# Optimization experiments

Hardware: AMD Instinct MI355X
Metric: run time of the kernel (lower is better)

The kernel has to match this reference:

```python
import jax, jax.numpy as jnp
import numpy as np

N = 40000          # spots (nodes)
G = 3000           # genes (input features)
C = 20             # num_classes
E = N * 16         # edges (avg degree 16)


def _uniform(key, shape, stdv):
    return jax.random.uniform(key, shape, jnp.float32, -stdv, stdv)


def _linear_params(key, n_in, n_out):
    # torch Linear default init: U(-1/sqrt(in), 1/sqrt(in)); stored as [in, out]
    k1, k2 = jax.random.split(key)
    s = 1.0 / np.sqrt(n_in)
    return _uniform(k1, (n_in, n_out), s), _uniform(k2, (n_out,), s)


def setup_inputs() -> dict:
    key = jax.random.key(0)
    ks = jax.random.split(key, 32)
    x = jax.random.normal(ks[0], (N, G), jnp.float32)
    adj_rows = jax.random.randint(ks[1], (E,), 0, N, jnp.int32)
    adj_cols = jax.random.randint(ks[2], (E,), 0, N, jnp.int32)
    adj_vals = jax.random.uniform(ks[3], (E,), jnp.float32)

    # GCN weights: GraphConvolution init U(-1/sqrt(out), 1/sqrt(out)), no bias
    def gcn_w(k, fi, fo):
        return _uniform(k, (fi, fo), 1.0 / np.sqrt(fo))

    inp = {
        "x": x, "adj_rows": adj_rows, "adj_cols": adj_cols, "adj_vals": adj_vals,
        "W1": gcn_w(ks[4], G, 512), "W2": gcn_w(ks[5], 512, 256),
        "W3": gcn_w(ks[6], 256, 128), "W4": gcn_w(ks[7], 128, 128),
        "W5": gcn_w(ks[8], 128, C),
    }
    # AE linear layers
    for name, (fi, fo), k in [
        ("enc1", (G, 512), ks[9]), ("enc2", (512, 256), ks[10]),
        ("enc3", (256, 128), ks[11]), ("zl", (128, 128), ks[12]),
        ("dec1", (128, 128), ks[13]), ("dec2", (128, 256), ks[14]),
        ("dec3", (256, 512), ks[15]), ("xbar", (512, G), ks[16]),
    ]:
        w, b = _linear_params(k, fi, fo)
        inp[name + "_w"], inp[name + "_b"] = w, b
    # Attention projection vectors (Linear(in_size, 1, bias=False))
    inp["a1"] = _uniform(ks[17], (512,), 1.0 / np.sqrt(512))
    inp["a2"] = _uniform(ks[18], (256,), 1.0 / np.sqrt(256))
    inp["a3"] = _uniform(ks[19], (128,), 1.0 / np.sqrt(128))
    inp["a4"] = _uniform(ks[20], (128,), 1.0 / np.sqrt(128))
    inp["scale"] = jax.random.normal(ks[21], (G,), jnp.float32)
    inp["additive"] = jax.random.normal(ks[22], (G,), jnp.float32)
    return inp


def _spmm(rows, cols, vals, dense, n):
    # out[r] = sum_e vals[e] * dense[cols[e]] for rows[e]==r  (sparse [n,n] @ dense)
    return jax.ops.segment_sum(vals[:, None] * dense[cols], rows, num_segments=n)


def _gcn(x, rows, cols, vals, W, n, active=True):
    out = _spmm(rows, cols, vals, x @ W, n)
    return jax.nn.relu(out) if active else out


def _attn(h, t, a):
    # stack two [N,D] branches, softmax over the branch axis, weighted sum
    z = jnp.stack([h, t], axis=1)           # [N,2,D]
    w = jnp.einsum('nbd,d->nb', z, a)        # [N,2]
    beta = jax.nn.softmax(w, axis=1)
    return jnp.einsum('nb,nbd->nd', beta, z)


def reference(x, adj_rows, adj_cols, adj_vals,
              W1, W2, W3, W4, W5,
              enc1_w, enc1_b, enc2_w, enc2_b, enc3_w, enc3_b, zl_w, zl_b,
              dec1_w, dec1_b, dec2_w, dec2_b, dec3_w, dec3_b, xbar_w, xbar_b,
              a1, a2, a3, a4, scale, additive):
    n = x.shape[0]
    # autoencoder
    t1 = jax.nn.relu(x @ enc1_w + enc1_b)
    t2 = jax.nn.relu(t1 @ enc2_w + enc2_b)
    t3 = jax.nn.relu(t2 @ enc3_w + enc3_b)
    z = t3 @ zl_w + zl_b
    d1 = jax.nn.relu(z @ dec1_w + dec1_b)
    d2 = jax.nn.relu(d1 @ dec2_w + dec2_b)
    d3 = jax.nn.relu(d2 @ dec3_w + dec3_b)
    x_bar = d3 @ xbar_w + xbar_b
    # GCN stack with attention-fused AE skip connections
    h = _gcn(x, adj_rows, adj_cols, adj_vals, W1, n)
    emb = _attn(h, t1, a1)
    h = _gcn(emb, adj_rows, adj_cols, adj_vals, W2, n)
    emb = _attn(h, t2, a2)
    h = _gcn(emb, adj_rows, adj_cols, adj_vals, W3, n)
    emb = _attn(h, t3, a3)
    h = _gcn(emb, adj_rows, adj_cols, adj_vals, W4, n)
    emb = _attn(h, z, a4)
    output = _gcn(emb, adj_rows, adj_cols, adj_vals, W5, n, active=False)
    return output, x_bar, jax.nn.sigmoid(scale), jnp.exp(additive)
```

## Files before the change

### kernel.cpp

```cpp
#include <hip/hip_runtime.h>
#include <cmath>

typedef unsigned short u16;
typedef unsigned int u32;
typedef __attribute__((ext_vector_type(8))) short short8;
typedef __attribute__((ext_vector_type(4))) short short4v;
typedef __attribute__((ext_vector_type(4))) float f32x4;

__device__ __forceinline__ float bf2f(u16 h) {
  union { u32 u; float f; } v; v.u = ((u32)h) << 16; return v.f;
}
__device__ __forceinline__ u16 f2bf(float f) {
  union { float f; u32 u; } v; v.f = f;
  u32 u = v.u;
  u32 r = (u + 0x7FFFu + ((u >> 16) & 1u)) >> 16;
  return (u16)r;
}

__global__ void convx_kernel(const float* __restrict__ x, u16* __restrict__ A0) {
  int idx = blockIdx.x * 256 + threadIdx.x;
  int r = blockIdx.y;
  if (idx >= 752) return;
  short4v o;
  if (r < 40000 && idx < 750) {
    float4 v = *(const float4*)(x + (size_t)r * 3000 + idx * 4);
    o[0] = (short)f2bf(v.x); o[1] = (short)f2bf(v.y);
    o[2] = (short)f2bf(v.z); o[3] = (short)f2bf(v.w);
  } else {
    o[0] = 0; o[1] = 0; o[2] = 0; o[3] = 0;
  }
  *(short4v*)(A0 + (size_t)r * 3008 + idx * 4) = o;
}

__global__ void convw_kernel(const float* __restrict__ W, u16* __restrict__ Wt,
                             int K, int N, int Kp) {
  int k = blockIdx.x * 256 + threadIdx.x;
  int n = blockIdx.y;
  if (k >= Kp) return;
  float v = (k < K && n < N) ? W[(size_t)k * N + n] : 0.f;
  Wt[(size_t)n * Kp + k] = f2bf(v);
}

__global__ void zero_kernel(int* p, int n) {
  int i = blockIdx.x * 256 + threadIdx.x;
  if (i < n) p[i] = 0;
}
__global__ void count_kernel(const int* __restrict__ rows, int* __restrict__ counts, int E) {
  int i = blockIdx.x * 256 + threadIdx.x;
  if (i < E) atomicAdd(&counts[rows[i]], 1);
}
__global__ __launch_bounds__(1024) void scan_kernel(const int* __restrict__ counts,
                                                    int* __restrict__ rowptr,
                                                    int* __restrict__ cursor, int n) {
  __shared__ int buf[1024];
  __shared__ int carry_s;
  int tid = threadIdx.x;
  if (tid == 0) carry_s = 0;
  __syncthreads();
  for (int base = 0; base < n; base += 1024) {
    int i = base + tid;
    int v = (i < n) ? counts[i] : 0;
    buf[tid] = v;
    __syncthreads();
    for (int off = 1; off < 1024; off <<= 1) {
      int tv = (tid >= off) ? buf[tid - off] : 0;
      __syncthreads();
      buf[tid] += tv;
      __syncthreads();
    }
    int incl = buf[tid];
    int carry = carry_s;
    if (i < n) { int ex = carry + incl - v; rowptr[i] = ex; cursor[i] = ex; }
    __syncthreads();
    if (tid == 1023) carry_s = carry + incl;
    __syncthreads();
  }
  if (tid == 0) rowptr[n] = carry_s;
}
__global__ void scatter_kernel(const int* __restrict__ rows, const int* __restrict__ cols,
                               const float* __restrict__ vals, int* __restrict__ cursor,
                               int* __restrict__ cols_s, float* __restrict__ vals_s, int E) {
  int i = blockIdx.x * 256 + threadIdx.x;
  if (i < E) {
    int r = rows[i];
    int p = atomicAdd(&cursor[r], 1);
    cols_s[p] = cols[i];
    vals_s[p] = vals[i];
  }
}

#define BM 128
#define BN 128
#define BK 32

template <bool BIAS, bool RELU, bool OUTBF16, int CH>
__global__ __launch_bounds__(256, 2) void gemm_bf16(
    const u16* __restrict__ A, int lda, const u16* __restrict__ Bt, int ldb,
    void* __restrict__ C1, int ldc,
    const float* __restrict__ bias, int M, int Nreal, int K, int MT, int NT) {
  __shared__ __align__(16) u16 As[2][BM * BK];
  __shared__ __align__(16) u16 Bs[2][BN * BK];
  const int lin = blockIdx.x;
  const int per = CH * NT;
  const int g = lin / per;
  const int r0 = lin - g * per;
  const int bx0 = g * CH;
  const int cw = min(CH, MT - bx0);
  const int bx = bx0 + r0 % cw;
  const int by = r0 / cw;

  const int tid = threadIdx.x;
  const int lane = tid & 63;
  const int wave = tid >> 6;
  const int mblk = bx * BM;
  const int nblk = by * BN;
  const int wm = (wave & 1) * 64;
  const int wn = (wave >> 1) * 64;
  const int ml = lane & 15;
  const int kg = lane >> 4;

  f32x4 acc[4][4];
#pragma unroll
  for (int i = 0; i < 4; ++i)
#pragma unroll
    for (int j = 0; j < 4; ++j) acc[i][j] = (f32x4)(0.f);

  const int nk = K / BK;
  const int sr = tid >> 2;
  const int sc = (tid & 3) * 8;
  const u16* gA0 = A + (size_t)(mblk + sr) * lda + sc;
  const u16* gA1 = A + (size_t)(mblk + sr + 64) * lda + sc;
  const u16* gB0 = Bt + (size_t)(nblk + sr) * ldb + sc;
  const u16* gB1 = Bt + (size_t)(nblk + sr + 64) * ldb + sc;

  auto stage = [&](int buf, int kt) {
    const int ko = kt * BK;
    u16* lA = &As[buf][0] + wave * 512;
    u16* lB = &Bs[buf][0] + wave * 512;
    __builtin_amdgcn_global_load_lds((const void*)(gA0 + ko), (void*)lA, 16, 0, 0);
    __builtin_amdgcn_global_load_lds((const void*)(gA1 + ko), (void*)(lA + 2048), 16, 0, 0);
    __builtin_amdgcn_global_load_lds((const void*)(gB0 + ko), (void*)lB, 16, 0, 0);
    __builtin_amdgcn_global_load_lds((const void*)(gB1 + ko), (void*)(lB + 2048), 16, 0, 0);
  };

  stage(0, 0);
  asm volatile("s_waitcnt vmcnt(0)" ::: "memory");
  __syncthreads();

  int cur = 0;
  for (int kt = 0; kt < nk; ++kt) {
    if (kt + 1 < nk) stage(cur ^ 1, kt + 1);
    short8 af[4], bfr[4];
#pragma unroll
    for (int i = 0; i < 4; ++i) {
      af[i] = *(const short8*)&As[cur][(wm + i * 16 + ml) * BK + kg * 8];
      bfr[i] = *(const short8*)&Bs[cur][(wn + i * 16 + ml) * BK + kg * 8];
    }
#pragma unroll
    for (int i = 0; i < 4; ++i)
#pragma unroll
      for (int j = 0; j < 4; ++j)
        acc[i][j] = __builtin_amdgcn_mfma_f32_16x16x32_bf16(af[i], bfr[j], acc[i][j], 0, 0, 0);
    asm volatile("s_waitcnt vmcnt(0)" ::: "memory");
    __syncthreads();
    cur ^= 1;
  }

#pragma unroll
  for (int i = 0; i < 4; ++i) {
    const int row0 = mblk + wm + i * 16 + kg * 4;
#pragma unroll
    for (int j = 0; j < 4; ++j) {
      const int col = nblk + wn + j * 16 + ml;
      if (col < Nreal) {
        float bv = BIAS ? bias[col] : 0.f;
#pragma unroll
        for (int r = 0; r < 4; ++r) {
          const int row = row0 + r;
          if (row < M) {
            float v = acc[i][j][r] + bv;
            if (RELU) v = fmaxf(v, 0.f);
            if (OUTBF16)
              ((u16*)C1)[(size_t)row * ldc + col] = f2bf(v);
            else
              ((float*)C1)[(size_t)row * ldc + col] = v;
          }
        }
      }
    }
  }
}

template <int MODE>
__global__ __launch_bounds__(512, 1) void gemm256p(
    const u16* __restrict__ A, int lda, const u16* __restrict__ Bt, int ldb,
    void* __restrict__ C1, void* __restrict__ C2, int ldc,
    const float* __restrict__ bias, int M, int Nreal, int K, int MT2, int NT) {
  __shared__ __align__(16) u16 smem[2 * 2 * 256 * 64];
  const int tid = threadIdx.x;
  const int lane = tid & 63;
  const int wave = tid >> 6;
  const int wm = wave >> 2;
  const int wn = wave & 3;
  const int ml = lane & 15;
  const int kg = lane >> 4;

  const int grp = blockIdx.x / (8 * NT);
  const int rr = blockIdx.x % (8 * NT);
  const int nb = min(8, MT2 - grp * 8);
  const int bx = grp * 8 + rr % nb;
  const int by = rr / nb;
  const int mblk = bx * 256;
  const int nblk = by * 256;

  f32x4 acc[8][4];
#pragma unroll
  for (int i = 0; i < 8; ++i)
#pragma unroll
    for (int j = 0; j < 4; ++j) acc[i][j] = (f32x4)(0.f);

  const int srow = tid >> 3;
  const int clog = (tid & 7) ^ (srow & 7);
  const size_t abase = (size_t)(mblk + srow) * lda + clog * 8;
  const size_t bbase = (size_t)(nblk + srow) * ldb + clog * 8;
  const int NKT = K / 64;

  auto stageA = [&](int d, int kt, int h) {
    u16* dst = smem + d * 16384 + h * 4096 + wave * 512;
    const u16* src = A + abase + (size_t)h * 64 * lda + kt * 64;
    __builtin_amdgcn_global_load_lds((const void*)src, (void*)dst, 16, 0, 0);
  };
  auto stageB = [&](int d, int kt, int h) {
    u16* dst = smem + 32768 + d * 16384 + h * 4096 + wave * 512;
    const u16* src = Bt + bbase + (size_t)h * 64 * ldb + kt * 64;
    __builtin_amdgcn_global_load_lds((const void*)src, (void*)dst, 16, 0, 0);
  };
  auto stageU0 = [&](int d, int kt) { stageB(d, kt, 0); stageB(d, kt, 1); };
  auto stageU1 = [&](int d, int kt) { stageB(d, kt, 2); stageB(d, kt, 3); };
  auto stageU2 = [&](int d, int kt) { stageA(d, kt, 0); stageA(d, kt, 2); };
  auto stageU3 = [&](int d, int kt) { stageA(d, kt, 1); stageA(d, kt, 3); };
  auto readA = [&](int d, int im, int kk) -> short8 {
    const int r = wm * 128 + im * 16 + ml;
    const int ch = (kk * 4 + kg) ^ (r & 7);
    return *(const short8*)&smem[d * 16384 + r * 64 + ch * 8];
  };
  auto readB = [&](int d, int j, int kk) -> short8 {
    const int r = wn * 64 + j * 16 + ml;
    const int ch = (kk * 4 + kg) ^ (r & 7);
    return *(const short8*)&smem[32768 + d * 16384 + r * 64 + ch * 8];
  };

  stageU0(0, 0); stageU1(0, 0); stageU2(0, 0); stageU3(0, 0);
  asm volatile("s_waitcnt vmcnt(2)" ::: "memory");
  __builtin_amdgcn_s_barrier();

  for (int kt = 0; kt < NKT; ++kt) {
    const int d = kt & 1;
    const bool more = (kt + 1 < NKT);
    short8 b[4][2];
#pragma unroll
    for (int j = 0; j < 4; ++j) { b[j][0] = readB(d, j, 0); b[j][1] = readB(d, j, 1); }
    {
      short8 a00 = readA(d, 0, 0), a01 = readA(d, 0, 1);
      short8 a10 = readA(d, 1, 0), a11 = readA(d, 1, 1);
      if (more) stageU0(d ^ 1, kt + 1);
      __builtin_amdgcn_s_setprio(1);
#pragma unroll
      for (int j = 0; j < 4; ++j) {
        acc[0][j] = __builtin_amdgcn_mfma_f32_16x16x32_bf16(a00, b[j][0], acc[0][j], 0, 0, 0);
        acc[1][j] = __builtin_amdgcn_mfma_f32_16x16x32_bf16(a10, b[j][0], acc[1][j], 0, 0, 0);
      }
#pragma unroll
      for (int j = 0; j < 4; ++j) {
        acc[0][j] = __builtin_amdgcn_mfma_f32_16x16x32_bf16(a01, b[j][1], acc[0][j], 0, 0, 0);
        acc[1][j] = __builtin_amdgcn_mfma_f32_16x16x32_bf16(a11, b[j][1], acc[1][j], 0, 0, 0);
      }
      __builtin_amdgcn_s_setprio(0);
    }
    {
      short8 a00 = readA(d, 2, 0), a01 = readA(d, 2, 1);
      short8 a10 = readA(d, 3, 0), a11 = readA(d, 3, 1);
      if (more) stageU1(d ^ 1, kt + 1);
      __builtin_amdgcn_s_setprio(1);
#pragma unroll
      for (int j = 0; j < 4; ++j) {
        acc[2][j] = __builtin_amdgcn_mfma_f32_16x16x32_bf16(a00, b[j][0], acc[2][j], 0, 0, 0);
        acc[3][j] = __builtin_amdgcn_mfma_f32_16x16x32_bf16(a10, b[j][0], acc[3][j], 0, 0, 0);
      }
#pragma unroll
      for (int j = 0; j < 4; ++j) {
        acc[2][j] = __builtin_amdgcn_mfma_f32_16x16x32_bf16(a01, b[j][1], acc[2][j], 0, 0, 0);
        acc[3][j] = __builtin_amdgcn_mfma_f32_16x16x32_bf16(a11, b[j][1], acc[3][j], 0, 0, 0);
      }
      __builtin_amdgcn_s_setprio(0);
    }
    if (more) asm volatile("s_waitcnt vmcnt(4)" ::: "memory");
    else      asm volatile("s_waitcnt vmcnt(0)" ::: "memory");
    __builtin_amdgcn_s_barrier();
    {
      short8 a00 = readA(d, 4, 0), a01 = readA(d, 4, 1);
      short8 a10 = readA(d, 5, 0), a11 = readA(d, 5, 1);
      if (more) stageU2(d ^ 1, kt + 1);
      __builtin_amdgcn_s_setprio(1);
#pragma unroll
      for (int j = 0; j < 4; ++j) {
        acc[4][j] = __builtin_amdgcn_mfma_f32_16x16x32_bf16(a00, b[j][0], acc[4][j], 0, 0, 0);
        acc[5][j] = __builtin_amdgcn_mfma_f32_16x16x32_bf16(a10, b[j][0], acc[5][j], 0, 0, 0);
      }
#pragma unroll
      for (int j = 0; j < 4; ++j) {
        acc[4][j] = __builtin_amdgcn_mfma_f32_16x16x32_bf16(a01, b[j][1], acc[4][j], 0, 0, 0);
        acc[5][j] = __builtin_amdgcn_mfma_f32_16x16x32_bf16(a11, b[j][1], acc[5][j], 0, 0, 0);
      }
      __builtin_amdgcn_s_setprio(0);
    }
    {
      short8 a00 = readA(d, 6, 0), a01 = readA(d, 6, 1);
      short8 a10 = readA(d, 7, 0), a11 = readA(d, 7, 1);
      if (more) stageU3(d ^ 1, kt + 1);
      __builtin_amdgcn_s_setprio(1);
#pragma unroll
      for (int j = 0; j < 4; ++j) {
        acc[6][j] = __builtin_amdgcn_mfma_f32_16x16x32_bf16(a00, b[j][0], acc[6][j], 0, 0, 0);
        acc[7][j] = __builtin_amdgcn_mfma_f32_16x16x32_bf16(a10, b[j][0], acc[7][j], 0, 0, 0);
      }
#pragma unroll
      for (int j = 0; j < 4; ++j) {
        acc[6][j] = __builtin_amdgcn_mfma_f32_16x16x32_bf16(a01, b[j][1], acc[6][j], 0, 0, 0);
        acc[7][j] = __builtin_amdgcn_mfma_f32_16x16x32_bf16(a11, b[j][1], acc[7][j], 0, 0, 0);
      }
      __builtin_amdgcn_s_setprio(0);
    }
    if (more) asm volatile("s_waitcnt vmcnt(2)" ::: "memory");
    __builtin_amdgcn_s_barrier();
  }

  __syncthreads();

  float* ep = (float*)smem;
  const int ES = 260;
  const int colg = nblk + lane * 4;
  const bool second = (MODE == 0) && (nblk >= 512);
  float bv0 = 0.f, bv1 = 0.f, bv2 = 0.f, bv3 = 0.f;
  if (MODE == 0) {
    if (!second) { float4 b4 = *(const float4*)(bias + colg); bv0 = b4.x; bv1 = b4.y; bv2 = b4.z; bv3 = b4.w; }
  } else {
    if (colg + 3 < Nreal) {
      float4 b4 = *(const float4*)(bias + colg);
      bv0 = b4.x; bv1 = b4.y; bv2 = b4.z; bv3 = b4.w;
    } else {
      if (colg + 0 < Nreal) bv0 = bias[colg + 0];
      if (colg + 1 < Nreal) bv1 = bias[colg + 1];
      if (colg + 2 < Nreal) bv2 = bias[colg + 2];
      if (colg + 3 < Nreal) bv3 = bias[colg + 3];
    }
  }
#pragma unroll
  for (int p = 0; p < 4; ++p) {
    if (p) __syncthreads();
    if (wm == (p >> 1)) {
#pragma unroll
      for (int ii = 0; ii < 4; ++ii) {
        const int i = (p & 1) * 4 + ii;
        const int lrow0 = ii * 16 + kg * 4;
#pragma unroll
        for (int j = 0; j < 4; ++j) {
          const int colL = wn * 64 + j * 16 + ml;
#pragma unroll
          for (int r = 0; r < 4; ++r) ep[(lrow0 + r) * ES + colL] = acc[i][j][r];
        }
      }
    }
    __syncthreads();
#pragma unroll
    for (int it = 0; it < 8; ++it) {
      const int lrow = wave * 8 + it;
      const int grow = mblk + p * 64 + lrow;
      if (grow < M) {
        float v0 = ep[lrow * ES + lane * 4 + 0] + bv0;
        float v1 = ep[lrow * ES + lane * 4 + 1] + bv1;
        float v2 = ep[lrow * ES + lane * 4 + 2] + bv2;
        float v3 = ep[lrow * ES + lane * 4 + 3] + bv3;
        if (MODE == 0) {
          if (!second) { v0 = fmaxf(v0, 0.f); v1 = fmaxf(v1, 0.f); v2 = fmaxf(v2, 0.f); v3 = fmaxf(v3, 0.f); }
          u16* dst = (second ? (u16*)C2 : (u16*)C1) + (size_t)grow * 512 + (second ? colg - 512 : colg);
          short4v o;
          o[0] = (short)f2bf(v0); o[1] = (short)f2bf(v1);
          o[2] = (short)f2bf(v2); o[3] = (short)f2bf(v3);
          *(short4v*)dst = o;
        } else {
          float* dst = (float*)C1 + (size_t)grow * ldc + colg;
          if (colg + 3 < Nreal) {
            float4 v; v.x = v0; v.y = v1; v.z = v2; v.w = v3;
            *(float4*)dst = v;
          } else {
            if (colg + 0 < Nreal) dst[0] = v0;
            if (colg + 1 < Nreal) dst[1] = v1;
            if (colg + 2 < Nreal) dst[2] = v2;
            if (colg + 3 < Nreal) dst[3] = v3;
          }
        }
      }
    }
  }
}

template <int D>
__global__ __launch_bounds__(256) void spmm_attn(const int* __restrict__ rowptr,
                                                 const int* __restrict__ colidx,
                                                 const float* __restrict__ vals,
                                                 const u16* __restrict__ X,
                                                 const u16* __restrict__ T,
                                                 const float* __restrict__ a,
                                                 u16* __restrict__ emb) {
  constexpr int VE = D / 64;
  const int wave = threadIdx.x >> 6, lane = threadIdx.x & 63;
  const int row = blockIdx.x * 4 + wave;
  const int co = lane * VE;
  float h[VE];
#pragma unroll
  for (int j = 0; j < VE; ++j) h[j] = 0.f;
  const int s = rowptr[row], e = rowptr[row + 1];
  for (int i = s; i < e; ++i) {
    const int c = colidx[i];
    const float v = vals[i];
    const u16* xr = X + (size_t)c * D + co;
    if constexpr (VE == 8) {
      short8 x8 = *(const short8*)xr;
#pragma unroll
      for (int j = 0; j < 8; ++j) h[j] += v * bf2f((u16)x8[j]);
    } else if constexpr (VE == 4) {
      short4v x4 = *(const short4v*)xr;
#pragma unroll
      for (int j = 0; j < 4; ++j) h[j] += v * bf2f((u16)x4[j]);
    } else {
      u32 x2 = *(const u32*)xr;
      h[0] += v * bf2f((u16)(x2 & 0xffffu));
      h[1] += v * bf2f((u16)(x2 >> 16));
    }
  }
#pragma unroll
  for (int j = 0; j < VE; ++j) h[j] = fmaxf(h[j], 0.f);

  float tv[VE];
  const u16* tr = T + (size_t)row * D + co;
  if constexpr (VE == 8) {
    short8 t8 = *(const short8*)tr;
#pragma unroll
    for (int j = 0; j < 8; ++j) tv[j] = bf2f((u16)t8[j]);
  } else if constexpr (VE == 4) {
    short4v t4 = *(const short4v*)tr;
#pragma unroll
    for (int j = 0; j < 4; ++j) tv[j] = bf2f((u16)t4[j]);
  } else {
    u32 t2 = *(const u32*)tr;
    tv[0] = bf2f((u16)(t2 & 0xffffu)); tv[1] = bf2f((u16)(t2 >> 16));
  }

  float wh = 0.f, wt = 0.f;
#pragma unroll
  for (int j = 0; j < VE; ++j) {
    float av = a[co + j];
    wh += av * h[j];
    wt += av * tv[j];
  }
  for (int off = 32; off; off >>= 1) {
    wh += __shfl_xor(wh, off);
    wt += __shfl_xor(wt, off);
  }
  float m = fmaxf(wh, wt);
  float e1 = expf(wh - m), e2 = expf(wt - m);
  float inv = 1.f / (e1 + e2);
  float b1 = e1 * inv, b2 = e2 * inv;
  u16* er = emb + (size_t)row * D + co;
  if constexpr (VE == 8) {
    short8 o;
#pragma unroll
    for (int j = 0; j < 8; ++j) o[j] = (short)f2bf(b1 * h[j] + b2 * tv[j]);
    *(short8*)er = o;
  } else if constexpr (VE == 4) {
    short4v o;
#pragma unroll
    for (int j = 0; j < 4; ++j) o[j] = (short)f2bf(b1 * h[j] + b2 * tv[j]);
    *(short4v*)er = o;
  } else {
    *(u32*)er = (u32)f2bf(b1 * h[0] + b2 * tv[0]) | ((u32)f2bf(b1 * h[1] + b2 * tv[1]) << 16);
  }
}

__global__ __launch_bounds__(64) void spmm_out_kernel(const int* __restrict__ rowptr,
                                                      const int* __restrict__ colidx,
                                                      const float* __restrict__ vals,
                                                      const u16* __restrict__ X,
                                                      float* __restrict__ Y) {
  int row = blockIdx.x;
  int c = threadIdx.x;
  float acc = 0.f;
  int s = rowptr[row], e = rowptr[row + 1];
  for (int i = s; i < e; ++i) {
    int col = colidx[i];
    float v = vals[i];
    if (c < 20) acc += v * bf2f(X[(size_t)col * 20 + c]);
  }
  if (c < 20) Y[(size_t)row * 20 + c] = acc;
}

__global__ __launch_bounds__(64) void xw5_kernel(const u16* __restrict__ emb,
                                                 const float* __restrict__ W5,
                                                 u16* __restrict__ xw5) {
  int row = blockIdx.x;
  int c = threadIdx.x;
  if (c >= 20) return;
  const short8* er = (const short8*)(emb + (size_t)row * 128);
  float acc = 0.f;
#pragma unroll
  for (int k8 = 0; k8 < 16; ++k8) {
    short8 v = er[k8];
#pragma unroll
    for (int j = 0; j < 8; ++j) acc += bf2f((u16)v[j]) * W5[(k8 * 8 + j) * 20 + c];
  }
  xw5[(size_t)row * 20 + c] = f2bf(acc);
}

__global__ void sig_exp_kernel(const float* __restrict__ scale, const float* __restrict__ additive,
                               float* __restrict__ osig, float* __restrict__ oexp, int g) {
  int i = blockIdx.x * 256 + threadIdx.x;
  if (i < g) {
    osig[i] = 1.f / (1.f + expf(-scale[i]));
    oexp[i] = expf(additive[i]);
  }
}

extern "C" void kernel_launch(void* const* d_in, const int* in_sizes, int n_in,
                              void* d_out, int out_size, void* d_ws, size_t ws_size,
                              hipStream_t stream) {
  (void)n_in; (void)out_size; (void)ws_size;
  const float* x      = (const float*)d_in[0];
  const int*   arows  = (const int*)d_in[1];
  const int*   acols  = (const int*)d_in[2];
  const float* avals  = (const float*)d_in[3];
  const float* W1     = (const float*)d_in[4];
  const float* W2     = (const float*)d_in[5];
  const float* W3     = (const float*)d_in[6];
  const float* W4     = (const float*)d_in[7];
  const float* W5     = (const float*)d_in[8];
  const float* enc1_w = (const float*)d_in[9],  *enc1_b = (const float*)d_in[10];
  const float* enc2_w = (const float*)d_in[11], *enc2_b = (const float*)d_in[12];
  const float* enc3_w = (const float*)d_in[13], *enc3_b = (const float*)d_in[14];
  const float* zl_w   = (const float*)d_in[15], *zl_b   = (const float*)d_in[16];
  const float* dec1_w = (const float*)d_in[17], *dec1_b = (const float*)d_in[18];
  const float* dec2_w = (const float*)d_in[19], *dec2_b = (const float*)d_in[20];
  const float* dec3_w = (const float*)d_in[21], *dec3_b = (const float*)d_in[22];
  const float* xbar_w = (const float*)d_in[23], *xbar_b = (const float*)d_in[24];
  const float* a1 = (const float*)d_in[25], *a2 = (const float*)d_in[26];
  const float* a3 = (const float*)d_in[27], *a4 = (const float*)d_in[28];
  const float* scale = (const float*)d_in[29], *additive = (const float*)d_in[30];

  const int E = in_sizes[1];
  const int N = 40000, G = 3000, Kx = 3008;
  const int Mp = 40192;

  float* out      = (float*)d_out;
  float* out_gcn  = out;
  float* out_xbar = out + (size_t)N * 20;
  float* out_sig  = out_xbar + (size_t)N * G;
  float* out_exp  = out_sig + G;

  char* wsb = (char*)d_ws;
  size_t off = 0;
  auto alloc = [&](size_t b) -> void* {
    void* p = wsb + off;
    off = (off + b + 255) & ~(size_t)255;
    return p;
  };
  u16* A0    = (u16*)alloc((size_t)Mp * Kx * 2);
  u16* t1    = (u16*)alloc((size_t)Mp * 512 * 2);
  u16* t2    = (u16*)alloc((size_t)Mp * 256 * 2);
  u16* t3    = (u16*)alloc((size_t)Mp * 128 * 2);
  u16* zb    = (u16*)alloc((size_t)Mp * 128 * 2);
  u16* dd1   = (u16*)alloc((size_t)Mp * 128 * 2);
  u16* dd2   = (u16*)alloc((size_t)Mp * 256 * 2);
  u16* dd3   = (u16*)alloc((size_t)Mp * 512 * 2);
  u16* xw    = (u16*)alloc((size_t)Mp * 512 * 2);
  u16* emb   = (u16*)alloc((size_t)Mp * 512 * 2);
  u16* xw5   = (u16*)alloc((size_t)N * 20 * 2);
  u16* catT  = (u16*)alloc((size_t)1024 * Kx * 2);
  u16* enc2T = (u16*)alloc((size_t)256 * 512 * 2);
  u16* enc3T = (u16*)alloc((size_t)128 * 256 * 2);
  u16* zlT   = (u16*)alloc((size_t)128 * 128 * 2);
  u16* dec1T = (u16*)alloc((size_t)128 * 128 * 2);
  u16* dec2T = (u16*)alloc((size_t)256 * 128 * 2);
  u16* dec3T = (u16*)alloc((size_t)512 * 256 * 2);
  u16* xbarT = (u16*)alloc((size_t)3072 * 512 * 2);
  u16* W2T   = (u16*)alloc((size_t)256 * 512 * 2);
  u16* W3T   = (u16*)alloc((size_t)128 * 256 * 2);
  u16* W4T   = (u16*)alloc((size_t)128 * 128 * 2);
  int* counts = (int*)alloc((size_t)N * 4);
  int* rowptr = (int*)alloc((size_t)(N + 1) * 4);
  int* cursor = (int*)alloc((size_t)N * 4);
  int* colss  = (int*)alloc((size_t)E * 4);
  float* valss = (float*)alloc((size_t)E * 4);

  convx_kernel<<<dim3(3, Mp), 256, 0, stream>>>(x, A0);
  auto convw = [&](const float* W, u16* Wt, int K, int Nw, int Kp, int Np) {
    convw_kernel<<<dim3((Kp + 255) / 256, Np), 256, 0, stream>>>(W, Wt, K, Nw, Kp);
  };
  convw(enc1_w, catT,             3000, 512, Kx, 512);
  convw(W1,     catT + 512 * Kx,  3000, 512, Kx, 512);
  convw(enc2_w, enc2T, 512, 256, 512, 256);
  convw(enc3_w, enc3T, 256, 128, 256, 128);
  convw(zl_w,   zlT,   128, 128, 128, 128);
  convw(dec1_w, dec1T, 128, 128, 128, 128);
  convw(dec2_w, dec2T, 128, 256, 128, 256);
  convw(dec3_w, dec3T, 256, 512, 256, 512);
  convw(xbar_w, xbarT, 512, 3000, 512, 3072);
  convw(W2,     W2T,   512, 256, 512, 256);
  convw(W3,     W3T,   256, 128, 256, 128);
  convw(W4,     W4T,   128, 128, 128, 128);

  zero_kernel<<<(N + 255) / 256, 256, 0, stream>>>(counts, N);
  count_kernel<<<(E + 255) / 256, 256, 0, stream>>>(arows, counts, E);
  scan_kernel<<<1, 1024, 0, stream>>>(counts, rowptr, cursor, N);
  scatter_kernel<<<(E + 255) / 256, 256, 0, stream>>>(arows, acols, avals, cursor, colss, valss, E);

  const int MT = 313;
  const int MT2 = 157;
  gemm256p<0><<<MT2 * 4, 512, 0, stream>>>(
      A0, Kx, catT, Kx, t1, xw, 512, enc1_b, N, 1024, Kx, MT2, 4);
  gemm_bf16<true, true, true, 32><<<MT * 2, 256, 0, stream>>>(
      t1, 512, enc2T, 512, t2, 256, enc2_b, N, 256, 512, MT, 2);
  gemm_bf16<true, true, true, 32><<<MT * 1, 256, 0, stream>>>(
      t2, 256, enc3T, 256, t3, 128, enc3_b, N, 128, 256, MT, 1);
  gemm_bf16<true, false, true, 32><<<MT * 1, 256, 0, stream>>>(
      t3, 128, zlT, 128, zb, 128, zl_b, N, 128, 128, MT, 1);
  gemm_bf16<true, true, true, 32><<<MT * 1, 256, 0, stream>>>(
      zb, 128, dec1T, 128, dd1, 128, dec1_b, N, 128, 128, MT, 1);
  gemm_bf16<true, true, true, 32><<<MT * 2, 256, 0, stream>>>(
      dd1, 128, dec2T, 128, dd2, 256, dec2_b, N, 256, 128, MT, 2);
  gemm_bf16<true, true, true, 32><<<MT * 4, 256, 0, stream>>>(
      dd2, 256, dec3T, 256, dd3, 512, dec3_b, N, 512, 256, MT, 4);
  gemm256p<1><<<MT2 * 12, 512, 0, stream>>>(
      dd3, 512, xbarT, 512, out_xbar, nullptr, 3000, xbar_b, N, 3000, 512, MT2, 12);

  spmm_attn<512><<<N / 4, 256, 0, stream>>>(rowptr, colss, valss, xw, t1, a1, emb);
  gemm_bf16<false, false, true, 32><<<MT * 2, 256, 0, stream>>>(
      emb, 512, W2T, 512, xw, 256, nullptr, N, 256, 512, MT, 2);
  spmm_attn<256><<<N / 4, 256, 0, stream>>>(rowptr, colss, valss, xw, t2, a2, emb);
  gemm_bf16<false, false, true, 32><<<MT * 1, 256, 0, stream>>>(
      emb, 256, W3T, 256, xw, 128, nullptr, N, 128, 256, MT, 1);
  spmm_attn<128><<<N / 4, 256, 0, stream>>>(rowptr, colss, valss, xw, t3, a3, emb);
  gemm_bf16<false, false, true, 32><<<MT * 1, 256, 0, stream>>>(
      emb, 128, W4T, 128, xw, 128, nullptr, N, 128, 128, MT, 1);
  spmm_attn<128><<<N / 4, 256, 0, stream>>>(rowptr, colss, valss, xw, zb, a4, emb);

  xw5_kernel<<<N, 64, 0, stream>>>(emb, W5, xw5);
  spmm_out_kernel<<<N, 64, 0, stream>>>(rowptr, colss, valss, xw5, out_gcn);

  sig_exp_kernel<<<(G + 255) / 256, 256, 0, stream>>>(scale, additive, out_sig, out_exp, G);
}
```

Before: 1.380 ms.

## Widen x conversion, wave-cooperative edge loads in SpMM, batch final-layer rows

The x-to-bf16 conversion now handles 8 elements per thread with two float4 loads and a 16-byte store, halving the grid width. In spmm_attn each wave loads up to 64 column indices and values at once with one coalesced load and broadcasts them with shuffles, instead of every lane reloading the same index and value for each edge. The final XW5 and output SpMM kernels now process 12 rows per 256-thread block, with W5 and the embedding rows staged in shared memory, replacing one 64-thread block per row in which most lanes sat idle. The aim is fewer redundant scalar loads and better thread utilisation, at the cost of shuffle overhead and extra shared-memory staging.

```diff
diff --git a/kernel.cpp b/kernel.cpp
--- a/kernel.cpp
+++ b/kernel.cpp
@@ -20,16 +20,21 @@
 __global__ void convx_kernel(const float* __restrict__ x, u16* __restrict__ A0) {
   int idx = blockIdx.x * 256 + threadIdx.x;
   int r = blockIdx.y;
-  if (idx >= 752) return;
-  short4v o;
-  if (r < 40000 && idx < 750) {
-    float4 v = *(const float4*)(x + (size_t)r * 3000 + idx * 4);
-    o[0] = (short)f2bf(v.x); o[1] = (short)f2bf(v.y);
-    o[2] = (short)f2bf(v.z); o[3] = (short)f2bf(v.w);
+  if (idx >= 376) return;
+  short8 o;
+  if (r < 40000 && idx < 375) {
+    const float* src = x + (size_t)r * 3000 + idx * 8;
+    float4 v0 = *(const float4*)src;
+    float4 v1 = *(const float4*)(src + 4);
+    o[0] = (short)f2bf(v0.x); o[1] = (short)f2bf(v0.y);
+    o[2] = (short)f2bf(v0.z); o[3] = (short)f2bf(v0.w);
+    o[4] = (short)f2bf(v1.x); o[5] = (short)f2bf(v1.y);
+    o[6] = (short)f2bf(v1.z); o[7] = (short)f2bf(v1.w);
   } else {
-    o[0] = 0; o[1] = 0; o[2] = 0; o[3] = 0;
-  }
-  *(short4v*)(A0 + (size_t)r * 3008 + idx * 4) = o;
+#pragma unroll
+    for (int j = 0; j < 8; ++j) o[j] = 0;
+  }
+  *(short8*)(A0 + (size_t)r * 3008 + idx * 8) = o;
 }
 
 __global__ void convw_kernel(const float* __restrict__ W, u16* __restrict__ Wt,
@@ -421,22 +426,27 @@
 #pragma unroll
   for (int j = 0; j < VE; ++j) h[j] = 0.f;
   const int s = rowptr[row], e = rowptr[row + 1];
-  for (int i = s; i < e; ++i) {
-    const int c = colidx[i];
-    const float v = vals[i];
-    const u16* xr = X + (size_t)c * D + co;
-    if constexpr (VE == 8) {
-      short8 x8 = *(const short8*)xr;
-#pragma unroll
-      for (int j = 0; j < 8; ++j) h[j] += v * bf2f((u16)x8[j]);
-    } else if constexpr (VE == 4) {
-      short4v x4 = *(const short4v*)xr;
-#pragma unroll
-      for (int j = 0; j < 4; ++j) h[j] += v * bf2f((u16)x4[j]);
-    } else {
-      u32 x2 = *(const u32*)xr;
-      h[0] += v * bf2f((u16)(x2 & 0xffffu));
-      h[1] += v * bf2f((u16)(x2 >> 16));
+  for (int base = s; base < e; base += 64) {
+    const int n = min(64, e - base);
+    int myc = 0; float myv = 0.f;
+    if (base + lane < e) { myc = colidx[base + lane]; myv = vals[base + lane]; }
+    for (int jj = 0; jj < n; ++jj) {
+      const int c = __shfl(myc, jj);
+      const float v = __shfl(myv, jj);
+      const u16* xr = X + (size_t)c * D + co;
+      if constexpr (VE == 8) {
+        short8 x8 = *(const short8*)xr;
+#pragma unroll
+        for (int j = 0; j < 8; ++j) h[j] += v * bf2f((u16)x8[j]);
+      } else if constexpr (VE == 4) {
+        short4v x4 = *(const short4v*)xr;
+#pragma unroll
+        for (int j = 0; j < 4; ++j) h[j] += v * bf2f((u16)x4[j]);
+      } else {
+        u32 x2 = *(const u32*)xr;
+        h[0] += v * bf2f((u16)(x2 & 0xffffu));
+        h[1] += v * bf2f((u16)(x2 >> 16));
+      }
     }
   }
 #pragma unroll
@@ -488,38 +498,58 @@
   }
 }
 
-__global__ __launch_bounds__(64) void spmm_out_kernel(const int* __restrict__ rowptr,
-                                                      const int* __restrict__ colidx,
-                                                      const float* __restrict__ vals,
-                                                      const u16* __restrict__ X,
-                                                      float* __restrict__ Y) {
-  int row = blockIdx.x;
-  int c = threadIdx.x;
+#define XROWS 12
+__global__ __launch_bounds__(256) void xw5_blk(const u16* __restrict__ emb,
+                                               const float* __restrict__ W5,
+                                               u16* __restrict__ xw5, int Nrow) {
+  __shared__ float W5s[128 * 20];
+  __shared__ u16 embs[XROWS * 128];
+  const int tid = threadIdx.x;
+  const int row0 = blockIdx.x * XROWS;
+  for (int i = tid; i < 2560; i += 256) W5s[i] = W5[i];
+  if (tid < 192) {
+    const int base = tid * 8;
+    const int grow = row0 + base / 128;
+    short8 v;
+    if (grow < Nrow) v = *(const short8*)(emb + (size_t)row0 * 128 + base);
+    else {
+#pragma unroll
+      for (int j = 0; j < 8; ++j) v[j] = 0;
+    }
+    *(short8*)(embs + base) = v;
+  }
+  __syncthreads();
+  const int r = tid / 20;
+  const int c = tid % 20;
+  if (r < XROWS && tid < 240) {
+    const int grow = row0 + r;
+    if (grow < Nrow) {
+      float acc = 0.f;
+#pragma unroll 8
+      for (int k = 0; k < 128; ++k) acc += bf2f(embs[r * 128 + k]) * W5s[k * 20 + c];
+      xw5[(size_t)grow * 20 + c] = f2bf(acc);
+    }
+  }
+}
+
+__global__ __launch_bounds__(256) void spmm_out_blk(const int* __restrict__ rowptr,
+                                                    const int* __restrict__ colidx,
+                                                    const float* __restrict__ vals,
+                                                    const u16* __restrict__ X,
+                                                    float* __restrict__ Y, int Nrow) {
+  const int tid = threadIdx.x;
+  const int r = tid / 20;
+  const int c = tid % 20;
+  if (r >= XROWS || tid >= 240) return;
+  const int row = blockIdx.x * XROWS + r;
+  if (row >= Nrow) return;
   float acc = 0.f;
-  int s = rowptr[row], e = rowptr[row + 1];
+  const int s = rowptr[row], e = rowptr[row + 1];
   for (int i = s; i < e; ++i) {
-    int col = colidx[i];
-    float v = vals[i];
-    if (c < 20) acc += v * bf2f(X[(size_t)col * 20 + c]);
-  }
-  if (c < 20) Y[(size_t)row * 20 + c] = acc;
-}
-
-__global__ __launch_bounds__(64) void xw5_kernel(const u16* __restrict__ emb,
-                                                 const float* __restrict__ W5,
-                                                 u16* __restrict__ xw5) {
-  int row = blockIdx.x;
-  int c = threadIdx.x;
-  if (c >= 20) return;
-  const short8* er = (const short8*)(emb + (size_t)row * 128);
-  float acc = 0.f;
-#pragma unroll
-  for (int k8 = 0; k8 < 16; ++k8) {
-    short8 v = er[k8];
-#pragma unroll
-    for (int j = 0; j < 8; ++j) acc += bf2f((u16)v[j]) * W5[(k8 * 8 + j) * 20 + c];
-  }
-  xw5[(size_t)row * 20 + c] = f2bf(acc);
+    const int col = colidx[i];
+    acc += vals[i] * bf2f(X[(size_t)col * 20 + c]);
+  }
+  Y[(size_t)row * 20 + c] = acc;
 }
 
 __global__ void sig_exp_kernel(const float* __restrict__ scale, const float* __restrict__ additive,
@@ -601,7 +631,7 @@
   int* colss  = (int*)alloc((size_t)E * 4);
   float* valss = (float*)alloc((size_t)E * 4);
 
-  convx_kernel<<<dim3(3, Mp), 256, 0, stream>>>(x, A0);
+  convx_kernel<<<dim3(2, Mp), 256, 0, stream>>>(x, A0);
   auto convw = [&](const float* W, u16* Wt, int K, int Nw, int Kp, int Np) {
     convw_kernel<<<dim3((Kp + 255) / 256, Np), 256, 0, stream>>>(W, Wt, K, Nw, Kp);
   };
@@ -653,8 +683,9 @@
       emb, 128, W4T, 128, xw, 128, nullptr, N, 128, 128, MT, 1);
   spmm_attn<128><<<N / 4, 256, 0, stream>>>(rowptr, colss, valss, xw, zb, a4, emb);
 
-  xw5_kernel<<<N, 64, 0, stream>>>(emb, W5, xw5);
-  spmm_out_kernel<<<N, 64, 0, stream>>>(rowptr, colss, valss, xw5, out_gcn);
+  const int XB = (N + XROWS - 1) / XROWS;
+  xw5_blk<<<XB, 256, 0, stream>>>(emb, W5, xw5, N);
+  spmm_out_blk<<<XB, 256, 0, stream>>>(rowptr, colss, valss, xw5, out_gcn, N);
 
   sig_exp_kernel<<<(G + 255) / 256, 256, 0, stream>>>(scale, additive, out_sig, out_exp, G);
 }
```

Measured after the change: 1.288 ms (median of 2 runs). 1.07x faster.
